# Performance work log

Hardware: AMD Instinct MI355X
Metric: run time of the kernel (lower is better)

## Reference

```python
import jax, jax.numpy as jnp
import numpy as np

B, S, D, H = 2, 2048, 1024, 16
HD = D // H  # head_dim = 64


def setup_inputs() -> dict:
    key = jax.random.key(0)
    ks = jax.random.split(key, 5)
    scale = 0.02
    x = jax.random.normal(ks[0], (B, S, D), dtype=jnp.float32)
    W_q = jax.random.normal(ks[1], (D, D), dtype=jnp.float32) * scale
    W_k = jax.random.normal(ks[2], (D, D), dtype=jnp.float32) * scale
    W_v = jax.random.normal(ks[3], (D, D), dtype=jnp.float32) * scale
    W_o = jax.random.normal(ks[4], (D, D), dtype=jnp.float32) * scale
    z = jnp.zeros((D,), dtype=jnp.float32)
    return {"x": x, "W_q": W_q, "b_q": z, "W_k": W_k, "b_k": z,
            "W_v": W_v, "b_v": z, "W_o": W_o, "b_o": z}


def _proj_heads(x, W, b):
    # [B,S,D] @ [D,D] -> [B,S,D] -> [B,H,S,HD]
    y = x @ W + b
    return y.reshape(x.shape[0], x.shape[1], H, HD).transpose(0, 2, 1, 3)


def reference(x, W_q, b_q, W_k, b_k, W_v, b_v, W_o, b_o):
    b, s, d = x.shape
    q = _proj_heads(x, W_q, b_q)  # [B,H,S,HD]
    k = _proj_heads(x, W_k, b_k)
    v = _proj_heads(x, W_v, b_v)
    scale = 1.0 / jnp.sqrt(jnp.float32(HD))
    # [B,H,S,S] causal scores
    scores = jnp.einsum('bhqe,bhke->bhqk', q, k) * scale
    causal = jnp.tril(jnp.ones((s, s), dtype=bool))
    scores = jnp.where(causal[None, None], scores, jnp.finfo(scores.dtype).min)
    attn = jax.nn.softmax(scores, axis=-1)
    ctx = jnp.einsum('bhqk,bhke->bhqe', attn, v)  # [B,H,S,HD]
    ctx = ctx.transpose(0, 2, 1, 3).reshape(b, s, d)
    return ctx @ W_o + b_o
```

## Files before the change

kernel.cpp:

```cpp
#include <hip/hip_runtime.h>
#include <hip/hip_bf16.h>
#include <math.h>


#define Bdim  2
#define Sdim  2048
#define Ddim  1024
#define Hn    16
#define HDdim 64
#define Mdim  (Bdim * Sdim)

#define QSCALE 0.18033688011112042f

typedef unsigned short ushort_t;
typedef __attribute__((ext_vector_type(8))) short bfrag;
typedef __attribute__((ext_vector_type(4))) float f4;

__device__ __forceinline__ ushort_t f2bf(float f) {
    union { float f; unsigned int i; } c;
    c.f = f;
    unsigned int x = c.i;
    unsigned int r = (x + 0x7fffu + ((x >> 16) & 1u)) >> 16;
    return (ushort_t)r;
}

__device__ __forceinline__ unsigned cvtpk(float lo, float hi) {
    unsigned r;
    asm("v_cvt_pk_bf16_f32 %0, %1, %2" : "=v"(r) : "v"(lo), "v"(hi));
    return r;
}

__device__ __forceinline__ void glds16(const void* g, void* l) {
    __builtin_amdgcn_global_load_lds(
        (const __attribute__((address_space(1))) unsigned int*)g,
        (__attribute__((address_space(3))) unsigned int*)l, 16, 0, 0);
}

__global__ __launch_bounds__(256)
void prep(const float* __restrict__ x, ushort_t* __restrict__ xb,
          const float* __restrict__ W0, const float* __restrict__ W1,
          const float* __restrict__ W2, const float* __restrict__ W3,
          ushort_t* __restrict__ qkvT, ushort_t* __restrict__ oT)
{
    __shared__ ushort_t t[64][72];
    const int tid = threadIdx.x;
    const int z = blockIdx.z;

    if (z >= 4) {
        size_t blk = (size_t)(z - 4) * 256 + blockIdx.y * 16 + blockIdx.x;
        size_t i = (blk * 256 + tid) * 8;
        float4 a = *(const float4*)(x + i);
        float4 b = *(const float4*)(x + i + 4);
        ushort_t o[8] = {f2bf(a.x), f2bf(a.y), f2bf(a.z), f2bf(a.w),
                         f2bf(b.x), f2bf(b.y), f2bf(b.z), f2bf(b.w)};
        *(bfrag*)(xb + i) = *(const bfrag*)o;
        return;
    }

    const float* W = (z == 0) ? W0 : (z == 1) ? W1 : (z == 2) ? W2 : W3;
    const int k0 = blockIdx.y * 64, n0 = blockIdx.x * 64;

    const int r = tid >> 4, c4 = (tid & 15) * 4;
    #pragma unroll
    for (int rr = 0; rr < 4; ++rr) {
        int k = r + rr * 16;
        float4 v = *(const float4*)&W[(size_t)(k0 + k) * Ddim + n0 + c4];
        t[c4 + 0][k] = f2bf(v.x);
        t[c4 + 1][k] = f2bf(v.y);
        t[c4 + 2][k] = f2bf(v.z);
        t[c4 + 3][k] = f2bf(v.w);
    }
    __syncthreads();
    ushort_t* out = (z < 3) ? (qkvT + (size_t)z * Ddim * Ddim) : oT;
    const int n = tid >> 2, kc = (tid & 3) * 16;
    *(bfrag*)&out[(size_t)(n0 + n) * Ddim + k0 + kc] = *(const bfrag*)&t[n][kc];
    *(bfrag*)&out[(size_t)(n0 + n) * Ddim + k0 + kc + 8] = *(const bfrag*)&t[n][kc + 8];
}

template <int MODE>
__global__ __launch_bounds__(256)
void gemm_mfma(const ushort_t* __restrict__ A, const ushort_t* __restrict__ Bt,
               const float* __restrict__ bQ, const float* __restrict__ bK,
               const float* __restrict__ bV,
               ushort_t* __restrict__ oQ, ushort_t* __restrict__ oK,
               ushort_t* __restrict__ oVt, float* __restrict__ oF)
{
    __shared__ ushort_t As[128 * 32];
    __shared__ ushort_t Bs[128 * 32];

    const int tid  = threadIdx.x;
    const int lane = tid & 63;
    const int w    = tid >> 6;
    const int l15  = lane & 15;
    const int quad = lane >> 4;
    const int wr   = w >> 1, wc = w & 1;
    const int m0 = blockIdx.y * 128;
    const int n0 = blockIdx.x * 128;

    f4 acc[4][4];
    #pragma unroll
    for (int i = 0; i < 4; ++i)
        #pragma unroll
        for (int j = 0; j < 4; ++j) acc[i][j] = (f4){0.f, 0.f, 0.f, 0.f};

    const int srow  = w * 32 + (lane >> 2);
    const int selem = (lane & 3) * 8;
    const ushort_t* gA = A  + (size_t)(m0 + srow) * Ddim + selem;
    const ushort_t* gB = Bt + (size_t)(n0 + srow) * Ddim + selem;
    char* lA0 = (char*)As + (w * 32) * 64;
    char* lB0 = (char*)Bs + (w * 32) * 64;

    for (int kk = 0; kk < Ddim; kk += 32) {
        __syncthreads();
        glds16(gA + kk,              lA0);
        glds16(gA + 16 * Ddim + kk,  lA0 + 1024);
        glds16(gB + kk,              lB0);
        glds16(gB + 16 * Ddim + kk,  lB0 + 1024);
        __syncthreads();

        bfrag Af[4], Bf[4];
        #pragma unroll
        for (int i = 0; i < 4; ++i)
            Af[i] = *(const bfrag*)&As[(wr * 64 + i * 16 + l15) * 32 + quad * 8];
        #pragma unroll
        for (int j = 0; j < 4; ++j)
            Bf[j] = *(const bfrag*)&Bs[(wc * 64 + j * 16 + l15) * 32 + quad * 8];
        #pragma unroll
        for (int i = 0; i < 4; ++i)
            #pragma unroll
            for (int j = 0; j < 4; ++j)
                acc[i][j] = __builtin_amdgcn_mfma_f32_16x16x32_bf16(Af[i], Bf[j], acc[i][j], 0, 0, 0);
    }

    if constexpr (MODE == 0) {
        const int sel   = n0 >> 10;
        const int dbase = n0 & 1023;
        const float* bias = (sel == 0) ? bQ : (sel == 1) ? bK : bV;
        ushort_t* dst = (sel == 0) ? oQ : (sel == 1) ? oK : oVt;
        #pragma unroll
        for (int j = 0; j < 4; ++j) {
            int dn = dbase + wc * 64 + j * 16 + l15;
            float bv = bias[dn];
            int h = dn >> 6, e = dn & 63;
            if (sel < 2) {
                #pragma unroll
                for (int i = 0; i < 4; ++i) {
                    #pragma unroll
                    for (int r = 0; r < 4; ++r) {
                        int m = m0 + wr * 64 + i * 16 + quad * 4 + r;
                        int b = m >> 11, s = m & 2047;
                        float v = acc[i][j][r] + bv;
                        if (sel == 0) v *= QSCALE;
                        dst[((((size_t)b * Hn + h) * Sdim + s) << 6) + e] = f2bf(v);
                    }
                }
            } else {
                #pragma unroll
                for (int i = 0; i < 4; ++i) {
                    #pragma unroll
                    for (int rp = 0; rp < 2; ++rp) {
                        int m = m0 + wr * 64 + i * 16 + quad * 4 + rp * 2;
                        int b = m >> 11, s = m & 2047;
                        unsigned pv = cvtpk(acc[i][j][rp * 2] + bv,
                                            acc[i][j][rp * 2 + 1] + bv);
                        *(unsigned*)&dst[(((size_t)b * Hn + h) * HDdim + e) * Sdim + s] = pv;
                    }
                }
            }
        }
    } else {
        #pragma unroll
        for (int j = 0; j < 4; ++j) {
            int n = n0 + wc * 64 + j * 16 + l15;
            float bv = bQ[n];
            #pragma unroll
            for (int i = 0; i < 4; ++i)
                #pragma unroll
                for (int r = 0; r < 4; ++r) {
                    int m = m0 + wr * 64 + i * 16 + quad * 4 + r;
                    oF[(size_t)m * Ddim + n] = acc[i][j][r] + bv;
                }
        }
    }
}

#define NBH (Bdim * Hn)

#define MFMA16(a, b, c) __builtin_amdgcn_mfma_f32_16x16x32_bf16(a, b, c, 0, 0, 0)
#define EXP2(x) __builtin_amdgcn_exp2f(x)

__global__ __launch_bounds__(256, 4)
void flash_mfma(const ushort_t* __restrict__ Q, const ushort_t* __restrict__ K,
                const ushort_t* __restrict__ Vt, ushort_t* __restrict__ ctx)
{
    __shared__ ushort_t KtS[2][64 * 64];
    __shared__ ushort_t VsS[2][64 * 64];
    __shared__ ushort_t PTS[4][1024];

    const int tid  = threadIdx.x;
    const int lane = tid & 63;
    const int w    = tid >> 6;
    const int l15  = lane & 15;
    const int quad = lane >> 4;

    const int qb = 31 - (blockIdx.x >> 5);
    const int bh = blockIdx.x & 31;
    const int q0 = qb * 64;
    const int qw = q0 + w * 16;
    const int ntiles = qb + 1;

    const ushort_t* Qrow = Q + ((size_t)bh * Sdim + qw + l15) * HDdim;
    const bfrag Qf0 = *(const bfrag*)(Qrow + quad * 8);
    const bfrag Qf1 = *(const bfrag*)(Qrow + 32 + quad * 8);

    const ushort_t* Kp = K  + (size_t)bh * Sdim * HDdim;
    const ushort_t* Vp = Vt + (size_t)bh * HDdim * Sdim;

    const int srow = w * 8 + (lane >> 3);
    const int scol = ((lane & 7) ^ (lane >> 3)) * 8;
    const ushort_t* gK = Kp + (size_t)srow * HDdim + scol;
    const ushort_t* gV = Vp + (size_t)srow * Sdim + scol;
    char* ldsK = (char*)KtS + w * 1024;
    char* ldsV = (char*)VsS + w * 1024;
    ushort_t* PTw = PTS[w];

    const int sw = l15 & 7;
    const int c0 = (quad ^ sw) << 4;
    const int c1 = c0 ^ 64;
    const char* KtR = (const char*)KtS + l15 * 128;
    const char* VsR = (const char*)VsS + l15 * 128;

    f4 O[4];
    #pragma unroll
    for (int c = 0; c < 4; ++c) O[c] = (f4){0.f, 0.f, 0.f, 0.f};
    float m_prev = -INFINITY, l_run = 0.f;

    glds16(gK,                       ldsK);
    glds16(gK + 32 * HDdim,          ldsK + 4096);
    glds16(gV,                       ldsV);
    glds16(gV + (size_t)32 * Sdim,   ldsV + 4096);
    __syncthreads();

    for (int kt = 0; kt < ntiles - 1; ++kt) {
        const int k0  = kt << 6;
        const int buf = kt & 1;
        const int nb  = buf ^ 1;

        {
            const size_t kn = (size_t)(k0 + 64);
            glds16(gK + kn * HDdim,               ldsK + nb * 8192);
            glds16(gK + (kn + 32) * HDdim,        ldsK + nb * 8192 + 4096);
            glds16(gV + kn,                       ldsV + nb * 8192);
            glds16(gV + kn + (size_t)32 * Sdim,   ldsV + nb * 8192 + 4096);
        }

        const char* Kb = KtR + buf * 8192;
        const char* Vb = VsR + buf * 8192;

        float p[4][4];
        #pragma unroll
        for (int h = 0; h < 4; ++h) {
            bfrag a0 = *(const bfrag*)(Kb + h * 2048 + c0);
            bfrag a1 = *(const bfrag*)(Kb + h * 2048 + c1);
            f4 s = (f4){0.f, 0.f, 0.f, 0.f};
            s = MFMA16(a0, Qf0, s);
            s = MFMA16(a1, Qf1, s);
            #pragma unroll
            for (int r = 0; r < 4; ++r) p[h][r] = s[r];
        }

        float mh0 = fmaxf(fmaxf(p[0][0], p[0][1]), fmaxf(p[0][2], p[0][3]));
        float mh1 = fmaxf(fmaxf(p[1][0], p[1][1]), fmaxf(p[1][2], p[1][3]));
        float mh2 = fmaxf(fmaxf(p[2][0], p[2][1]), fmaxf(p[2][2], p[2][3]));
        float mh3 = fmaxf(fmaxf(p[3][0], p[3][1]), fmaxf(p[3][2], p[3][3]));
        float mt = fmaxf(fmaxf(mh0, mh1), fmaxf(mh2, mh3));
        mt = fmaxf(mt, __shfl_xor(mt, 16, 64));
        mt = fmaxf(mt, __shfl_xor(mt, 32, 64));

        if (__any(mt > m_prev + 8.f)) {
            float m_new = fmaxf(m_prev, mt);
            float alpha = EXP2(m_prev - m_new);
            l_run *= alpha;
            #pragma unroll
            for (int r = 0; r < 4; ++r) {
                float ar = __shfl(alpha, (lane & 48) + quad * 4 + r, 64);
                #pragma unroll
                for (int c = 0; c < 4; ++c) O[c][r] *= ar;
            }
            m_prev = m_new;
        }

        float rs0 = 0.f, rs1 = 0.f, rs2 = 0.f, rs3 = 0.f;
        #pragma unroll
        for (int r = 0; r < 4; ++r) {
            p[0][r] = EXP2(p[0][r] - m_prev); rs0 += p[0][r];
            p[1][r] = EXP2(p[1][r] - m_prev); rs1 += p[1][r];
            p[2][r] = EXP2(p[2][r] - m_prev); rs2 += p[2][r];
            p[3][r] = EXP2(p[3][r] - m_prev); rs3 += p[3][r];
        }
        float rsum = (rs0 + rs1) + (rs2 + rs3);
        rsum += __shfl_xor(rsum, 16, 64);
        rsum += __shfl_xor(rsum, 32, 64);
        l_run += rsum;

        #pragma unroll
        for (int h = 0; h < 4; ++h) {
            uint2 pw;
            pw.x = cvtpk(p[h][0], p[h][1]);
            pw.y = cvtpk(p[h][2], p[h][3]);
            *(uint2*)&PTw[((((h << 1) + (quad >> 1)) * 16 + l15) << 3) + (quad & 1) * 4] = pw;
        }
        bfrag pA0 = *(const bfrag*)&PTw[lane * 8];
        bfrag pA1 = *(const bfrag*)&PTw[512 + lane * 8];

        #pragma unroll
        for (int c = 0; c < 4; ++c) {
            bfrag v0 = *(const bfrag*)(Vb + c * 2048 + c0);
            bfrag v1 = *(const bfrag*)(Vb + c * 2048 + c1);
            O[c] = MFMA16(pA0, v0, O[c]);
            O[c] = MFMA16(pA1, v1, O[c]);
        }

        __syncthreads();
    }

    {
        const int buf = (ntiles - 1) & 1;
        const char* Kb = KtR + buf * 8192;
        const char* Vb = VsR + buf * 8192;

        float p[4][4];
        float mt = -INFINITY;
        #pragma unroll
        for (int h = 0; h < 4; ++h) {
            if (h <= w) {
                bfrag a0 = *(const bfrag*)(Kb + h * 2048 + c0);
                bfrag a1 = *(const bfrag*)(Kb + h * 2048 + c1);
                f4 s = (f4){0.f, 0.f, 0.f, 0.f};
                s = MFMA16(a0, Qf0, s);
                s = MFMA16(a1, Qf1, s);
                if (h == w) {
                    #pragma unroll
                    for (int r = 0; r < 4; ++r) {
                        float v = (quad * 4 + r <= l15) ? s[r] : -INFINITY;
                        p[h][r] = v;
                        mt = fmaxf(mt, v);
                    }
                } else {
                    #pragma unroll
                    for (int r = 0; r < 4; ++r) {
                        p[h][r] = s[r];
                        mt = fmaxf(mt, s[r]);
                    }
                }
            } else {
                #pragma unroll
                for (int r = 0; r < 4; ++r) p[h][r] = -INFINITY;
            }
        }
        mt = fmaxf(mt, __shfl_xor(mt, 16, 64));
        mt = fmaxf(mt, __shfl_xor(mt, 32, 64));

        if (__any(mt > m_prev + 8.f)) {
            float m_new = fmaxf(m_prev, mt);
            float alpha = EXP2(m_prev - m_new);
            l_run *= alpha;
            #pragma unroll
            for (int r = 0; r < 4; ++r) {
                float ar = __shfl(alpha, (lane & 48) + quad * 4 + r, 64);
                #pragma unroll
                for (int c = 0; c < 4; ++c) O[c][r] *= ar;
            }
            m_prev = m_new;
        }

        float rsum = 0.f;
        #pragma unroll
        for (int h = 0; h < 4; ++h)
            #pragma unroll
            for (int r = 0; r < 4; ++r) {
                float e = EXP2(p[h][r] - m_prev);
                p[h][r] = e;
                rsum += e;
            }
        rsum += __shfl_xor(rsum, 16, 64);
        rsum += __shfl_xor(rsum, 32, 64);
        l_run += rsum;

        #pragma unroll
        for (int h = 0; h < 4; ++h) {
            uint2 pw;
            pw.x = cvtpk(p[h][0], p[h][1]);
            pw.y = cvtpk(p[h][2], p[h][3]);
            *(uint2*)&PTw[((((h << 1) + (quad >> 1)) * 16 + l15) << 3) + (quad & 1) * 4] = pw;
        }
        bfrag pA0 = *(const bfrag*)&PTw[lane * 8];
        #pragma unroll
        for (int c = 0; c < 4; ++c) {
            bfrag v0 = *(const bfrag*)(Vb + c * 2048 + c0);
            O[c] = MFMA16(pA0, v0, O[c]);
        }
        if (w >= 2) {
            bfrag pA1 = *(const bfrag*)&PTw[512 + lane * 8];
            #pragma unroll
            for (int c = 0; c < 4; ++c) {
                bfrag v1 = *(const bfrag*)(Vb + c * 2048 + c1);
                O[c] = MFMA16(pA1, v1, O[c]);
            }
        }
    }

    const int b = bh >> 4, h = bh & 15;
    #pragma unroll
    for (int r = 0; r < 4; ++r) {
        float inv_l = 1.0f / __shfl(l_run, (lane & 48) + quad * 4 + r, 64);
        size_t base = ((size_t)b * Sdim + qw + quad * 4 + r) * Ddim + h * HDdim + l15;
        #pragma unroll
        for (int c = 0; c < 4; ++c)
            ctx[base + c * 16] = f2bf(O[c][r] * inv_l);
    }
}

extern "C" void kernel_launch(void* const* d_in, const int* in_sizes, int n_in,
                              void* d_out, int out_size, void* d_ws, size_t ws_size,
                              hipStream_t stream)
{
    const int NX = Mdim * Ddim;
    const int NW = Ddim * Ddim;
    int xi = 0, wi[4] = {1, 3, 5, 7}, bi[4] = {2, 4, 6, 8}, nw = 0, nb = 0;
    bool sized = true;
    for (int i = 0; i < 9; ++i) {
        if (in_sizes[i] == NX) xi = i;
        else if (in_sizes[i] == NW) { if (nw < 4) wi[nw++] = i; }
        else if (in_sizes[i] == Ddim) { if (nb < 4) bi[nb++] = i; }
        else sized = false;
    }
    int iWq, iWk, iWv, iWo, ibq, ibk, ibv, ibo;
    if (!sized || xi == 0) {
        xi = 0; iWq = 1; ibq = 2; iWk = 3; ibk = 4; iWv = 5; ibv = 6; iWo = 7; ibo = 8;
    } else {
        iWk = wi[0]; iWo = wi[1]; iWq = wi[2]; iWv = wi[3];
        ibk = bi[0]; ibo = bi[1]; ibq = bi[2]; ibv = bi[3];
    }

    const float* x  = (const float*)d_in[xi];
    const float* Wq = (const float*)d_in[iWq];
    const float* bq = (const float*)d_in[ibq];
    const float* Wk = (const float*)d_in[iWk];
    const float* bk = (const float*)d_in[ibk];
    const float* Wv = (const float*)d_in[iWv];
    const float* bv = (const float*)d_in[ibv];
    const float* Wo = (const float*)d_in[iWo];
    const float* bo = (const float*)d_in[ibo];
    float* out = (float*)d_out;

    const size_t elems = (size_t)Mdim * Ddim;
    const size_t welems = (size_t)Ddim * Ddim;
    ushort_t* Qb    = (ushort_t*)d_ws;
    ushort_t* Kb    = Qb + elems;
    ushort_t* Vtb   = Kb + elems;
    ushort_t* Cb    = Vtb + elems;
    ushort_t* xb    = Cb + elems;
    ushort_t* qkvT  = xb + elems;
    ushort_t* WoT   = qkvT + 3 * welems;

    dim3 blk(256);
    prep<<<dim3(16, 16, 12), blk, 0, stream>>>(x, xb, Wq, Wk, Wv, Wo, qkvT, WoT);

    gemm_mfma<0><<<dim3(3 * Ddim / 128, Mdim / 128), blk, 0, stream>>>(
        xb, qkvT, bq, bk, bv, Qb, Kb, Vtb, nullptr);

    flash_mfma<<<dim3(32 * NBH), blk, 0, stream>>>(Qb, Kb, Vtb, Cb);

    gemm_mfma<1><<<dim3(Ddim / 128, Mdim / 128), blk, 0, stream>>>(
        Cb, WoT, bo, nullptr, nullptr, nullptr, nullptr, nullptr, out);
}
```

Measured before the change: 189.2 us.

## Double flash attention query tile to 128 rows with 8 waves per block

The flash attention kernel now processes 128 query rows per block with 512 threads (8 waves), so each K/V tile loaded into shared memory is reused by twice as many waves. Each thread issues one async load per tile instead of two. The diagonal handling is split: one tile gets masked inside the loop for the first four waves, and the final tile is processed only by the upper four waves. This halves the grid size and the global K/V traffic, at the cost of bigger blocks, more wasted work on the masked diagonal, and fewer blocks for balancing the causal workload.

Result: slower. 194.9 us (+3.0%).

```diff
diff --git a/kernel.cpp b/kernel.cpp
--- a/kernel.cpp
+++ b/kernel.cpp
@@ -189,13 +189,13 @@
 #define MFMA16(a, b, c) __builtin_amdgcn_mfma_f32_16x16x32_bf16(a, b, c, 0, 0, 0)
 #define EXP2(x) __builtin_amdgcn_exp2f(x)
 
-__global__ __launch_bounds__(256, 4)
+__global__ __launch_bounds__(512, 4)
 void flash_mfma(const ushort_t* __restrict__ Q, const ushort_t* __restrict__ K,
                 const ushort_t* __restrict__ Vt, ushort_t* __restrict__ ctx)
 {
     __shared__ ushort_t KtS[2][64 * 64];
     __shared__ ushort_t VsS[2][64 * 64];
-    __shared__ ushort_t PTS[4][1024];
+    __shared__ ushort_t PTS[8][1024];
 
     const int tid  = threadIdx.x;
     const int lane = tid & 63;
@@ -203,11 +203,11 @@
     const int l15  = lane & 15;
     const int quad = lane >> 4;
 
-    const int qb = 31 - (blockIdx.x >> 5);
+    const int qb = 15 - (blockIdx.x >> 5);
     const int bh = blockIdx.x & 31;
-    const int q0 = qb * 64;
+    const int q0 = qb * 128;
     const int qw = q0 + w * 16;
-    const int ntiles = qb + 1;
+    const int ntiles = 2 * qb + 2;
 
     const ushort_t* Qrow = Q + ((size_t)bh * Sdim + qw + l15) * HDdim;
     const bfrag Qf0 = *(const bfrag*)(Qrow + quad * 8);
@@ -216,8 +216,8 @@
     const ushort_t* Kp = K  + (size_t)bh * Sdim * HDdim;
     const ushort_t* Vp = Vt + (size_t)bh * HDdim * Sdim;
 
-    const int srow = w * 8 + (lane >> 3);
-    const int scol = ((lane & 7) ^ (lane >> 3)) * 8;
+    const int srow = tid >> 3;
+    const int scol = ((tid & 7) ^ ((tid >> 3) & 7)) * 8;
     const ushort_t* gK = Kp + (size_t)srow * HDdim + scol;
     const ushort_t* gV = Vp + (size_t)srow * Sdim + scol;
     char* ldsK = (char*)KtS + w * 1024;
@@ -235,10 +235,8 @@
     for (int c = 0; c < 4; ++c) O[c] = (f4){0.f, 0.f, 0.f, 0.f};
     float m_prev = -INFINITY, l_run = 0.f;
 
-    glds16(gK,                       ldsK);
-    glds16(gK + 32 * HDdim,          ldsK + 4096);
-    glds16(gV,                       ldsV);
-    glds16(gV + (size_t)32 * Sdim,   ldsV + 4096);
+    glds16(gK, ldsK);
+    glds16(gV, ldsV);
     __syncthreads();
 
     for (int kt = 0; kt < ntiles - 1; ++kt) {
@@ -248,98 +246,179 @@
 
         {
             const size_t kn = (size_t)(k0 + 64);
-            glds16(gK + kn * HDdim,               ldsK + nb * 8192);
-            glds16(gK + (kn + 32) * HDdim,        ldsK + nb * 8192 + 4096);
-            glds16(gV + kn,                       ldsV + nb * 8192);
-            glds16(gV + kn + (size_t)32 * Sdim,   ldsV + nb * 8192 + 4096);
+            glds16(gK + kn * HDdim, ldsK + nb * 8192);
+            glds16(gV + kn,         ldsV + nb * 8192);
         }
 
         const char* Kb = KtR + buf * 8192;
         const char* Vb = VsR + buf * 8192;
 
-        float p[4][4];
-        #pragma unroll
-        for (int h = 0; h < 4; ++h) {
-            bfrag a0 = *(const bfrag*)(Kb + h * 2048 + c0);
-            bfrag a1 = *(const bfrag*)(Kb + h * 2048 + c1);
-            f4 s = (f4){0.f, 0.f, 0.f, 0.f};
-            s = MFMA16(a0, Qf0, s);
-            s = MFMA16(a1, Qf1, s);
-            #pragma unroll
-            for (int r = 0; r < 4; ++r) p[h][r] = s[r];
-        }
-
-        float mh0 = fmaxf(fmaxf(p[0][0], p[0][1]), fmaxf(p[0][2], p[0][3]));
-        float mh1 = fmaxf(fmaxf(p[1][0], p[1][1]), fmaxf(p[1][2], p[1][3]));
-        float mh2 = fmaxf(fmaxf(p[2][0], p[2][1]), fmaxf(p[2][2], p[2][3]));
-        float mh3 = fmaxf(fmaxf(p[3][0], p[3][1]), fmaxf(p[3][2], p[3][3]));
-        float mt = fmaxf(fmaxf(mh0, mh1), fmaxf(mh2, mh3));
-        mt = fmaxf(mt, __shfl_xor(mt, 16, 64));
-        mt = fmaxf(mt, __shfl_xor(mt, 32, 64));
-
-        if (__any(mt > m_prev + 8.f)) {
-            float m_new = fmaxf(m_prev, mt);
-            float alpha = EXP2(m_prev - m_new);
-            l_run *= alpha;
-            #pragma unroll
-            for (int r = 0; r < 4; ++r) {
-                float ar = __shfl(alpha, (lane & 48) + quad * 4 + r, 64);
-                #pragma unroll
-                for (int c = 0; c < 4; ++c) O[c][r] *= ar;
-            }
-            m_prev = m_new;
-        }
-
-        float rs0 = 0.f, rs1 = 0.f, rs2 = 0.f, rs3 = 0.f;
-        #pragma unroll
-        for (int r = 0; r < 4; ++r) {
-            p[0][r] = EXP2(p[0][r] - m_prev); rs0 += p[0][r];
-            p[1][r] = EXP2(p[1][r] - m_prev); rs1 += p[1][r];
-            p[2][r] = EXP2(p[2][r] - m_prev); rs2 += p[2][r];
-            p[3][r] = EXP2(p[3][r] - m_prev); rs3 += p[3][r];
-        }
-        float rsum = (rs0 + rs1) + (rs2 + rs3);
-        rsum += __shfl_xor(rsum, 16, 64);
-        rsum += __shfl_xor(rsum, 32, 64);
-        l_run += rsum;
-
-        #pragma unroll
-        for (int h = 0; h < 4; ++h) {
-            uint2 pw;
-            pw.x = cvtpk(p[h][0], p[h][1]);
-            pw.y = cvtpk(p[h][2], p[h][3]);
-            *(uint2*)&PTw[((((h << 1) + (quad >> 1)) * 16 + l15) << 3) + (quad & 1) * 4] = pw;
-        }
-        bfrag pA0 = *(const bfrag*)&PTw[lane * 8];
-        bfrag pA1 = *(const bfrag*)&PTw[512 + lane * 8];
-
-        #pragma unroll
-        for (int c = 0; c < 4; ++c) {
-            bfrag v0 = *(const bfrag*)(Vb + c * 2048 + c0);
-            bfrag v1 = *(const bfrag*)(Vb + c * 2048 + c1);
-            O[c] = MFMA16(pA0, v0, O[c]);
-            O[c] = MFMA16(pA1, v1, O[c]);
-        }
-
-        __syncthreads();
-    }
-
-    {
-        const int buf = (ntiles - 1) & 1;
-        const char* Kb = KtR + buf * 8192;
-        const char* Vb = VsR + buf * 8192;
-
-        float p[4][4];
-        float mt = -INFINITY;
-        #pragma unroll
-        for (int h = 0; h < 4; ++h) {
-            if (h <= w) {
+        if (kt < 2 * qb) {
+            float p[4][4];
+            #pragma unroll
+            for (int h = 0; h < 4; ++h) {
                 bfrag a0 = *(const bfrag*)(Kb + h * 2048 + c0);
                 bfrag a1 = *(const bfrag*)(Kb + h * 2048 + c1);
                 f4 s = (f4){0.f, 0.f, 0.f, 0.f};
                 s = MFMA16(a0, Qf0, s);
                 s = MFMA16(a1, Qf1, s);
-                if (h == w) {
+                #pragma unroll
+                for (int r = 0; r < 4; ++r) p[h][r] = s[r];
+            }
+
+            float mh0 = fmaxf(fmaxf(p[0][0], p[0][1]), fmaxf(p[0][2], p[0][3]));
+            float mh1 = fmaxf(fmaxf(p[1][0], p[1][1]), fmaxf(p[1][2], p[1][3]));
+            float mh2 = fmaxf(fmaxf(p[2][0], p[2][1]), fmaxf(p[2][2], p[2][3]));
+            float mh3 = fmaxf(fmaxf(p[3][0], p[3][1]), fmaxf(p[3][2], p[3][3]));
+            float mt = fmaxf(fmaxf(mh0, mh1), fmaxf(mh2, mh3));
+            mt = fmaxf(mt, __shfl_xor(mt, 16, 64));
+            mt = fmaxf(mt, __shfl_xor(mt, 32, 64));
+
+            if (__any(mt > m_prev + 8.f)) {
+                float m_new = fmaxf(m_prev, mt);
+                float alpha = EXP2(m_prev - m_new);
+                l_run *= alpha;
+                #pragma unroll
+                for (int r = 0; r < 4; ++r) {
+                    float ar = __shfl(alpha, (lane & 48) + quad * 4 + r, 64);
+                    #pragma unroll
+                    for (int c = 0; c < 4; ++c) O[c][r] *= ar;
+                }
+                m_prev = m_new;
+            }
+
+            float rs0 = 0.f, rs1 = 0.f, rs2 = 0.f, rs3 = 0.f;
+            #pragma unroll
+            for (int r = 0; r < 4; ++r) {
+                p[0][r] = EXP2(p[0][r] - m_prev); rs0 += p[0][r];
+                p[1][r] = EXP2(p[1][r] - m_prev); rs1 += p[1][r];
+                p[2][r] = EXP2(p[2][r] - m_prev); rs2 += p[2][r];
+                p[3][r] = EXP2(p[3][r] - m_prev); rs3 += p[3][r];
+            }
+            float rsum = (rs0 + rs1) + (rs2 + rs3);
+            rsum += __shfl_xor(rsum, 16, 64);
+            rsum += __shfl_xor(rsum, 32, 64);
+            l_run += rsum;
+
+            #pragma unroll
+            for (int h = 0; h < 4; ++h) {
+                uint2 pw;
+                pw.x = cvtpk(p[h][0], p[h][1]);
+                pw.y = cvtpk(p[h][2], p[h][3]);
+                *(uint2*)&PTw[((((h << 1) + (quad >> 1)) * 16 + l15) << 3) + (quad & 1) * 4] = pw;
+            }
+            bfrag pA0 = *(const bfrag*)&PTw[lane * 8];
+            bfrag pA1 = *(const bfrag*)&PTw[512 + lane * 8];
+
+            #pragma unroll
+            for (int c = 0; c < 4; ++c) {
+                bfrag v0 = *(const bfrag*)(Vb + c * 2048 + c0);
+                bfrag v1 = *(const bfrag*)(Vb + c * 2048 + c1);
+                O[c] = MFMA16(pA0, v0, O[c]);
+                O[c] = MFMA16(pA1, v1, O[c]);
+            }
+        } else {
+            float p[4][4];
+            float mt = -INFINITY;
+            #pragma unroll
+            for (int h = 0; h < 4; ++h) {
+                if (h <= w) {
+                    bfrag a0 = *(const bfrag*)(Kb + h * 2048 + c0);
+                    bfrag a1 = *(const bfrag*)(Kb + h * 2048 + c1);
+                    f4 s = (f4){0.f, 0.f, 0.f, 0.f};
+                    s = MFMA16(a0, Qf0, s);
+                    s = MFMA16(a1, Qf1, s);
+                    if (h == w) {
+                        #pragma unroll
+                        for (int r = 0; r < 4; ++r) {
+                            float v = (quad * 4 + r <= l15) ? s[r] : -INFINITY;
+                            p[h][r] = v;
+                            mt = fmaxf(mt, v);
+                        }
+                    } else {
+                        #pragma unroll
+                        for (int r = 0; r < 4; ++r) {
+                            p[h][r] = s[r];
+                            mt = fmaxf(mt, s[r]);
+                        }
+                    }
+                } else {
+                    #pragma unroll
+                    for (int r = 0; r < 4; ++r) p[h][r] = -INFINITY;
+                }
+            }
+            mt = fmaxf(mt, __shfl_xor(mt, 16, 64));
+            mt = fmaxf(mt, __shfl_xor(mt, 32, 64));
+
+            if (__any(mt > m_prev + 8.f)) {
+                float m_new = fmaxf(m_prev, mt);
+                float alpha = EXP2(m_prev - m_new);
+                l_run *= alpha;
+                #pragma unroll
+                for (int r = 0; r < 4; ++r) {
+                    float ar = __shfl(alpha, (lane & 48) + quad * 4 + r, 64);
+                    #pragma unroll
+                    for (int c = 0; c < 4; ++c) O[c][r] *= ar;
+                }
+                m_prev = m_new;
+            }
+
+            float rsum = 0.f;
+            #pragma unroll
+            for (int h = 0; h < 4; ++h)
+                #pragma unroll
+                for (int r = 0; r < 4; ++r) {
+                    float e = EXP2(p[h][r] - m_prev);
+                    p[h][r] = e;
+                    rsum += e;
+                }
+            rsum += __shfl_xor(rsum, 16, 64);
+            rsum += __shfl_xor(rsum, 32, 64);
+            l_run += rsum;
+
+            #pragma unroll
+            for (int h = 0; h < 4; ++h) {
+                uint2 pw;
+                pw.x = cvtpk(p[h][0], p[h][1]);
+                pw.y = cvtpk(p[h][2], p[h][3]);
+                *(uint2*)&PTw[((((h << 1) + (quad >> 1)) * 16 + l15) << 3) + (quad & 1) * 4] = pw;
+            }
+            bfrag pA0 = *(const bfrag*)&PTw[lane * 8];
+            #pragma unroll
+            for (int c = 0; c < 4; ++c) {
+                bfrag v0 = *(const bfrag*)(Vb + c * 2048 + c0);
+                O[c] = MFMA16(pA0, v0, O[c]);
+            }
+            if (w >= 2) {
+                bfrag pA1 = *(const bfrag*)&PTw[512 + lane * 8];
+                #pragma unroll
+                for (int c = 0; c < 4; ++c) {
+                    bfrag v1 = *(const bfrag*)(Vb + c * 2048 + c1);
+                    O[c] = MFMA16(pA1, v1, O[c]);
+                }
+            }
+        }
+
+        __syncthreads();
+    }
+
+    if (w >= 4) {
+        const int buf = (ntiles - 1) & 1;
+        const char* Kb = KtR + buf * 8192;
+        const char* Vb = VsR + buf * 8192;
+
+        float p[4][4];
+        float mt = -INFINITY;
+        #pragma unroll
+        for (int h = 0; h < 4; ++h) {
+            const int g = 4 + h;
+            if (g <= w) {
+                bfrag a0 = *(const bfrag*)(Kb + h * 2048 + c0);
+                bfrag a1 = *(const bfrag*)(Kb + h * 2048 + c1);
+                f4 s = (f4){0.f, 0.f, 0.f, 0.f};
+                s = MFMA16(a0, Qf0, s);
+                s = MFMA16(a1, Qf1, s);
+                if (g == w) {
                     #pragma unroll
                     for (int r = 0; r < 4; ++r) {
                         float v = (quad * 4 + r <= l15) ? s[r] : -INFINITY;
@@ -400,7 +479,7 @@
             bfrag v0 = *(const bfrag*)(Vb + c * 2048 + c0);
             O[c] = MFMA16(pA0, v0, O[c]);
         }
-        if (w >= 2) {
+        if (w >= 6) {
             bfrag pA1 = *(const bfrag*)&PTw[512 + lane * 8];
             #pragma unroll
             for (int c = 0; c < 4; ++c) {
@@ -470,7 +549,7 @@
     gemm_mfma<0><<<dim3(3 * Ddim / 128, Mdim / 128), blk, 0, stream>>>(
         xb, qkvT, bq, bk, bv, Qb, Kb, Vtb, nullptr);
 
-    flash_mfma<<<dim3(32 * NBH), blk, 0, stream>>>(Qb, Kb, Vtb, Cb);
+    flash_mfma<<<dim3(16 * NBH), dim3(512), 0, stream>>>(Qb, Kb, Vtb, Cb);
 
     gemm_mfma<1><<<dim3(Ddim / 128, Mdim / 128), blk, 0, stream>>>(
         Cb, WoT, bo, nullptr, nullptr, nullptr, nullptr, nullptr, out);
```
